# Kernel tuning notes

Measured on AMD Instinct MI355X. Metric: run time of the kernel, lower is better.

## Reference

```python
import jax, jax.numpy as jnp
import numpy as np

INF = 1.0e6  # sentinel distance for rows/cols with no background pixel


def _edt(mask):
    """Exact 2D Euclidean distance transform.

    For each pixel of mask [B,C,H,W], returns the Euclidean distance to the
    nearest pixel where mask == 0 (scipy.ndimage.distance_transform_edt
    semantics: nonzero = foreground, zero = background/feature).
    Uses the separable 2-pass algorithm: 1D distance along H, then an exact
    min over parabolas along W (done as a vectorized scan over column index).
    """
    B, C, H, W = mask.shape
    is_fg = mask != 0  # [B,C,H,W]

    # ---- pass 1: 1D distance along axis H to nearest zero in same column ----
    fg_h = jnp.moveaxis(is_fg, 2, 0)  # [H,B,C,W]

    def run_step(d, fg_row):  # d: [B,C,W]
        d = jnp.where(fg_row, d + 1.0, 0.0)
        return d, d

    init = jnp.full((B, C, W), INF, jnp.float32)
    _, d_fwd = jax.lax.scan(run_step, init, fg_h)
    _, d_bwd = jax.lax.scan(run_step, init, fg_h, reverse=True)
    g = jnp.minimum(jnp.minimum(d_fwd, d_bwd), INF)  # [H,B,C,W]
    f = jnp.moveaxis(g * g, 0, 2)  # [B,C,H,W] squared vertical distance

    # ---- pass 2: D[...,j] = min_k (j-k)^2 + f[...,k]  (exact 2D sq. EDT) ----
    js = jnp.arange(W, dtype=jnp.float32)  # [W]
    f_k = jnp.moveaxis(f, 3, 0)  # [W,B,C,H]

    def min_step(D, xs):
        k, fk = xs  # scalar, [B,C,H]
        cand = (js - k) ** 2 + fk[..., None]  # [B,C,H,W]
        return jnp.minimum(D, cand), None

    D0 = jnp.full((B, C, H, W), INF * INF, jnp.float32)
    D, _ = jax.lax.scan(min_step, D0, (js, f_k))
    return jnp.sqrt(D)


def setup_inputs() -> dict:
    key = jax.random.key(0)
    k1, k2 = jax.random.split(key)
    B, C, H, W = 16, 1, 512, 512
    output = jax.random.normal(k1, (B, C, H, W), dtype=jnp.float32)
    target = jax.random.randint(k2, (B, C, H, W), 0, 2, dtype=jnp.int32)
    return {"output": output, "target": target}


def reference(output, target):
    prob = jax.nn.sigmoid(output)  # [B,C,H,W]
    tgt = target.astype(jnp.float32)
    # signed distance: distance inside foreground minus distance inside background
    dist = _edt(1.0 - tgt) - _edt(tgt)  # [B,C,H,W]
    return jnp.mean(prob * dist)
```

## Files before the change

kernel.cpp:

```cpp
#include <hip/hip_runtime.h>
#include <math.h>

#define HDIM 512
#define WDIM 512
#define SEG 16
#define SROWS 32
#define VCOLS 32
#define VTHREADS 512
#define ROWS_PB 8
#define HTHREADS 256
#define INF_I (1 << 20)
#define ENC_SENT 127


__global__ __launch_bounds__(VTHREADS) void vert_pass6(const int* __restrict__ tgt,
                                                       signed char* __restrict__ sdist) {
    __shared__ int s_fs1[SEG][VCOLS], s_ls1[SEG][VCOLS];
    __shared__ int s_fs0[SEG][VCOLS], s_ls0[SEG][VCOLS];
    __shared__ int s_c1f[SEG][VCOLS], s_c1b[SEG][VCOLS];
    __shared__ int s_c0f[SEG][VCOLS], s_c0b[SEG][VCOLS];

    int tid = threadIdx.x;
    int w = tid & (VCOLS - 1);
    int seg = tid >> 5;
    int bW = WDIM / VCOLS;
    int b = blockIdx.x / bW;
    int wbase = (blockIdx.x % bW) * VCOLS;
    size_t colbase = (size_t)b * HDIM * WDIM + wbase + w;
    const int* col = tgt + colbase + (size_t)(seg * SROWS) * WDIM;

    unsigned R1 = 0u;
    #pragma unroll 8
    for (int h = 0; h < SROWS; ++h) {
        int tv = col[(size_t)h * WDIM];
        R1 |= ((unsigned)(tv != 0)) << h;
    }
    unsigned R0 = ~R1;

    s_fs1[seg][w] = R1 ? __builtin_ctz(R1) : SROWS;
    s_ls1[seg][w] = R1 ? 31 - __builtin_clz(R1) : -1;
    s_fs0[seg][w] = R0 ? __builtin_ctz(R0) : SROWS;
    s_ls0[seg][w] = R0 ? 31 - __builtin_clz(R0) : -1;
    __syncthreads();

    if (tid < 128) {
        int cw = tid & (VCOLS - 1);
        int md = tid >> 5;
        int c = INF_I;
        if (md == 0) {
            for (int s = 0; s < SEG; ++s) {
                s_c1f[s][cw] = c;
                int ls = s_ls1[s][cw];
                c = (ls >= 0) ? (SROWS - 1 - ls) : c + SROWS;
            }
        } else if (md == 1) {
            for (int s = SEG - 1; s >= 0; --s) {
                s_c1b[s][cw] = c;
                int fs = s_fs1[s][cw];
                c = (fs < SROWS) ? fs : c + SROWS;
            }
        } else if (md == 2) {
            for (int s = 0; s < SEG; ++s) {
                s_c0f[s][cw] = c;
                int ls = s_ls0[s][cw];
                c = (ls >= 0) ? (SROWS - 1 - ls) : c + SROWS;
            }
        } else {
            for (int s = SEG - 1; s >= 0; --s) {
                s_c0b[s][cw] = c;
                int fs = s_fs0[s][cw];
                c = (fs < SROWS) ? fs : c + SROWS;
            }
        }
    }
    __syncthreads();

    int c1f = s_c1f[seg][w], c1b = s_c1b[seg][w];
    int c0f = s_c0f[seg][w], c0b = s_c0b[seg][w];

    signed char* os = sdist + colbase + (size_t)(seg * SROWS) * WDIM;

    unsigned mle = 0u;
    for (int h = 0; h < SROWS; ++h) {
        mle = (mle << 1) | 1u;
        unsigned a1 = R1 & mle;
        int d1f = a1 ? (h - (31 - __builtin_clz(a1))) : c1f + h + 1;
        unsigned b1 = R1 >> h;
        int d1b = b1 ? __builtin_ctz(b1) : c1b + (SROWS - h);
        int g1 = min(d1f, d1b);
        unsigned a0 = R0 & mle;
        int d0f = a0 ? (h - (31 - __builtin_clz(a0))) : c0f + h + 1;
        unsigned b0 = R0 >> h;
        int d0b = b0 ? __builtin_ctz(b0) : c0b + (SROWS - h);
        int g0 = min(d0f, d0b);

        signed char sval = ((R1 >> h) & 1u) ? (signed char)(-min(g0, ENC_SENT))
                                            : (signed char)min(g1, ENC_SENT);
        os[(size_t)h * WDIM] = sval;
    }
}

__global__ __launch_bounds__(HTHREADS) void horiz_pass6(const int* __restrict__ sdist4,
                                                        const float* __restrict__ outp,
                                                        double* __restrict__ partial) {
    __shared__ float sf[ROWS_PB * WDIM];
    __shared__ double swave[4];

    int tid = threadIdx.x;
    size_t base = (size_t)blockIdx.x * (ROWS_PB * WDIM);

    const int* sp = sdist4 + base / 4;
    for (int i = tid; i < (ROWS_PB * WDIM) / 4; i += HTHREADS) {
        int p = sp[i];
        int j = i * 4;
        #pragma unroll
        for (int k = 0; k < 4; ++k) {
            int sv = (p << (24 - 8 * k)) >> 24;
            int neg = sv < 0;
            int e = neg ? -sv : sv;
            float g = (e >= ENC_SENT) ? 1.0e6f : (float)e;
            float f = g * g;
            sf[j + k] = neg ? -f : f;
        }
    }
    __syncthreads();

    double local = 0.0;
    for (int idx = tid; idx < ROWS_PB * WDIM; idx += HTHREADS) {
        int row = idx >> 9;
        int j = idx & (WDIM - 1);
        const float* env = sf + row * WDIM;
        float sj = env[j];
        float sgn = (sj > 0.0f) ? 1.0f : -1.0f;
        float best = fabsf(sj);
        for (int rad = 1; rad < WDIM; ++rad) {
            float rr = (float)(rad * rad);
            if (rr >= best) break;
            int kl = j - rad; kl = kl < 0 ? 0 : kl;
            int kr = j + rad; kr = kr > WDIM - 1 ? WDIM - 1 : kr;
            float cl = rr + fmaxf(sgn * env[kl], 0.0f);
            float cr = rr + fmaxf(sgn * env[kr], 0.0f);
            best = fminf(best, fminf(cl, cr));
        }
        float dist = sgn * sqrtf(best);
        float x = outp[base + idx];
        float prob = 1.0f / (1.0f + expf(-x));
        local += (double)(prob * dist);
    }

    double v = local;
    #pragma unroll
    for (int off = 32; off > 0; off >>= 1) v += __shfl_down(v, off, 64);
    int wid = tid >> 6, lane = tid & 63;
    if (lane == 0) swave[wid] = v;
    __syncthreads();
    if (tid == 0) partial[blockIdx.x] = swave[0] + swave[1] + swave[2] + swave[3];
}

__global__ __launch_bounds__(256) void finalize6(const double* __restrict__ partial,
                                                 float* __restrict__ out,
                                                 int npart, double invN) {
    __shared__ double swave[4];
    int tid = threadIdx.x;
    double local = 0.0;
    for (int i = tid; i < npart; i += 256) local += partial[i];
    #pragma unroll
    for (int off = 32; off > 0; off >>= 1) local += __shfl_down(local, off, 64);
    int wid = tid >> 6, lane = tid & 63;
    if (lane == 0) swave[wid] = local;
    __syncthreads();
    if (tid == 0) out[0] = (float)((swave[0] + swave[1] + swave[2] + swave[3]) * invN);
}

extern "C" void kernel_launch(void* const* d_in, const int* in_sizes, int n_in,
                              void* d_out, int out_size, void* d_ws, size_t ws_size,
                              hipStream_t stream) {
    const float* outp = (const float*)d_in[0];
    const int* tgt = (const int*)d_in[1];
    int N = in_sizes[0];
    int B = N / (HDIM * WDIM);

    int npart = (B * HDIM) / ROWS_PB;

    double* partial = (double*)((char*)d_ws + 256);
    signed char* sdist = (signed char*)((char*)d_ws + 32768);

    vert_pass6<<<B * (WDIM / VCOLS), VTHREADS, 0, stream>>>(tgt, sdist);
    horiz_pass6<<<npart, HTHREADS, 0, stream>>>((const int*)sdist, outp, partial);
    finalize6<<<1, 256, 0, stream>>>(partial, (float*)d_out, npart, 1.0 / (double)N);
}
```

Measured before the change: 31.83 us.

## Split horizontal envelope into per-class padded arrays and unroll the radius search

```diff
diff --git a/kernel.cpp b/kernel.cpp
--- a/kernel.cpp
+++ b/kernel.cpp
@@ -7,13 +7,15 @@
 #define SROWS 32
 #define VCOLS 32
 #define VTHREADS 512
-#define ROWS_PB 8
+#define ROWS_PB 4
 #define HTHREADS 256
+#define PAD 32
+#define LROW (WDIM + 2 * PAD)
 #define INF_I (1 << 20)
 #define ENC_SENT 127
 
 
-__global__ __launch_bounds__(VTHREADS) void vert_pass6(const int* __restrict__ tgt,
+__global__ __launch_bounds__(VTHREADS) void vert_pass7(const int* __restrict__ tgt,
                                                        signed char* __restrict__ sdist) {
     __shared__ int s_fs1[SEG][VCOLS], s_ls1[SEG][VCOLS];
     __shared__ int s_fs0[SEG][VCOLS], s_ls0[SEG][VCOLS];
@@ -100,19 +102,28 @@
     }
 }
 
-__global__ __launch_bounds__(HTHREADS) void horiz_pass6(const int* __restrict__ sdist4,
+__global__ __launch_bounds__(HTHREADS) void horiz_pass7(const int* __restrict__ sdist4,
                                                         const float* __restrict__ outp,
                                                         double* __restrict__ partial) {
-    __shared__ float sf[ROWS_PB * WDIM];
+    __shared__ float sf1[ROWS_PB * LROW];
+    __shared__ float sf0[ROWS_PB * LROW];
     __shared__ double swave[4];
 
     int tid = threadIdx.x;
     size_t base = (size_t)blockIdx.x * (ROWS_PB * WDIM);
+
+    for (int i = tid; i < ROWS_PB * LROW; i += HTHREADS) {
+        int c = i % LROW;
+        if (c < PAD || c >= PAD + WDIM) { sf1[i] = 3.0e12f; sf0[i] = 3.0e12f; }
+    }
+    __syncthreads();
 
     const int* sp = sdist4 + base / 4;
     for (int i = tid; i < (ROWS_PB * WDIM) / 4; i += HTHREADS) {
         int p = sp[i];
         int j = i * 4;
+        int row = j >> 9;
+        int lbase = row * LROW + PAD + (j & (WDIM - 1));
         #pragma unroll
         for (int k = 0; k < 4; ++k) {
             int sv = (p << (24 - 8 * k)) >> 24;
@@ -120,7 +131,8 @@
             int e = neg ? -sv : sv;
             float g = (e >= ENC_SENT) ? 1.0e6f : (float)e;
             float f = g * g;
-            sf[j + k] = neg ? -f : f;
+            sf1[lbase + k] = neg ? 0.0f : f;
+            sf0[lbase + k] = neg ? f : 0.0f;
         }
     }
     __syncthreads();
@@ -129,21 +141,35 @@
     for (int idx = tid; idx < ROWS_PB * WDIM; idx += HTHREADS) {
         int row = idx >> 9;
         int j = idx & (WDIM - 1);
-        const float* env = sf + row * WDIM;
-        float sj = env[j];
-        float sgn = (sj > 0.0f) ? 1.0f : -1.0f;
-        float best = fabsf(sj);
-        for (int rad = 1; rad < WDIM; ++rad) {
+        float x = outp[base + idx];
+        const float* e1 = sf1 + row * LROW + PAD;
+        const float* e0 = sf0 + row * LROW + PAD;
+        int cls0 = e1[j] > 0.0f;
+        const float* env = cls0 ? e1 : e0;
+        float best = env[j];
+
+        for (int rad = 1; rad <= PAD - 3; rad += 4) {
             float rr = (float)(rad * rad);
             if (rr >= best) break;
-            int kl = j - rad; kl = kl < 0 ? 0 : kl;
-            int kr = j + rad; kr = kr > WDIM - 1 ? WDIM - 1 : kr;
-            float cl = rr + fmaxf(sgn * env[kl], 0.0f);
-            float cr = rr + fmaxf(sgn * env[kr], 0.0f);
-            best = fminf(best, fminf(cl, cr));
-        }
-        float dist = sgn * sqrtf(best);
-        float x = outp[base + idx];
+            #pragma unroll
+            for (int q = 0; q < 4; ++q) {
+                int r2 = rad + q;
+                float rrq = (float)(r2 * r2);
+                best = fminf(best, fminf(rrq + env[j - r2], rrq + env[j + r2]));
+            }
+        }
+        if (best > (float)((PAD + 1) * (PAD + 1))) {
+            for (int rad = PAD + 1; rad < WDIM; ++rad) {
+                float rr = (float)(rad * rad);
+                if (rr >= best) break;
+                int kl = j - rad; kl = kl < 0 ? 0 : kl;
+                int kr = j + rad; kr = kr > WDIM - 1 ? WDIM - 1 : kr;
+                best = fminf(best, fminf(rr + env[kl], rr + env[kr]));
+            }
+        }
+
+        float sd = sqrtf(best);
+        float dist = cls0 ? sd : -sd;
         float prob = 1.0f / (1.0f + expf(-x));
         local += (double)(prob * dist);
     }
@@ -157,7 +183,7 @@
     if (tid == 0) partial[blockIdx.x] = swave[0] + swave[1] + swave[2] + swave[3];
 }
 
-__global__ __launch_bounds__(256) void finalize6(const double* __restrict__ partial,
+__global__ __launch_bounds__(256) void finalize7(const double* __restrict__ partial,
                                                  float* __restrict__ out,
                                                  int npart, double invN) {
     __shared__ double swave[4];
@@ -185,7 +211,7 @@
     double* partial = (double*)((char*)d_ws + 256);
     signed char* sdist = (signed char*)((char*)d_ws + 32768);
 
-    vert_pass6<<<B * (WDIM / VCOLS), VTHREADS, 0, stream>>>(tgt, sdist);
-    horiz_pass6<<<npart, HTHREADS, 0, stream>>>((const int*)sdist, outp, partial);
-    finalize6<<<1, 256, 0, stream>>>(partial, (float*)d_out, npart, 1.0 / (double)N);
-}
+    vert_pass7<<<B * (WDIM / VCOLS), VTHREADS, 0, stream>>>(tgt, sdist);
+    horiz_pass7<<<npart, HTHREADS, 0, stream>>>((const int*)sdist, outp, partial);
+    finalize7<<<1, 256, 0, stream>>>(partial, (float*)d_out, npart, 1.0 / (double)N);
+}
```

Measured after the change: 32.21 us. No clear change (+1.2%).
